# Kernel tuning notes

Hardware: AMD Instinct MI355X
Metric: run time of the kernel (lower is better)

Reference implementation:

```python
import jax, jax.numpy as jnp
import numpy as np

# Model dims (match init_kwargs / input_specs)
T, N, E, F_IN, F_OUT, BW = 16, 50000, 131072, 64, 64, 3


def setup_inputs() -> dict:
    key = jax.random.key(0)
    ks = jax.random.split(key, 6)
    x = jax.random.normal(ks[0], (T, N, F_IN), dtype=jnp.float32)
    M = jax.random.normal(ks[1], (T, T), dtype=jnp.float32)
    adj_rows = jax.random.randint(ks[2], (T, E), 0, N, dtype=jnp.int32)
    adj_cols = jax.random.randint(ks[3], (T, E), 0, N, dtype=jnp.int32)
    adj_vals = jax.random.uniform(ks[4], (T, E), dtype=jnp.float32)
    lim = float(np.sqrt(6.0 / (F_IN + F_OUT)))  # xavier_uniform
    weight = jax.random.uniform(ks[5], (F_IN, F_OUT), minval=-lim, maxval=lim, dtype=jnp.float32)
    return {"x": x, "M": M, "adj_vals": adj_vals, "weight": weight,
            "adj_rows": adj_rows, "adj_cols": adj_cols}


def _spmm(vals, rows, cols, x):
    # COO sparse [N,N] @ dense [N,F]: gather source rows, scatter-add to dest rows.
    return jax.ops.segment_sum(vals[:, None] * x[cols], rows, num_segments=x.shape[0])


def reference(x, M, adj_vals, weight, adj_rows, adj_cols):
    Tn, Nn, F = x.shape
    # Xt = M @ X (full M, as in compute_AtXt)
    Xt = (M @ x.reshape(Tn, -1)).reshape(Tn, Nn, F)
    k_idx = jnp.arange(Tn)
    AtXt = jnp.zeros((Tn, Nn, F), dtype=x.dtype)
    # Banded combination: At[k] = sum_{d=0}^{BW-1, k-d>=0} M[k, k-d] * A[k-d]
    # so At[k] @ Xt[k] = sum_d M[k,k-d] * (A[k-d] @ Xt[k])  -- avoids materializing At.
    for d in range(BW):
        j = k_idx - d
        valid = j >= 0
        jc = jnp.maximum(j, 0)
        w = jnp.where(valid, M[k_idx, jc], 0.0)  # [T] banded weights
        contrib = jax.vmap(_spmm)(adj_vals[jc], adj_rows[jc], adj_cols[jc], Xt)  # [T,N,F]
        AtXt = AtXt + w[:, None, None] * contrib
    # dropout is identity in eval mode; final dense projection
    return AtXt @ weight  # [T, N, F_OUT]
```

## Files before the change

### kernel.cpp

```cpp
#include <hip/hip_runtime.h>

#define TT 16
#define NN 50000
#define FF 64
#define EE 131072
#define NEDGE (TT*EE)
#define RPB 32
#define NRANGE ((NN + RPB - 1) / RPB)
#define NSUB 8
#define BCAP 256
#define NBUCK (NRANGE*NSUB)
#define SLOTS (NSUB*BCAP)
#define EMAX 1791
#define TAILI (EMAX*2)

typedef __attribute__((ext_vector_type(8))) short bf16x8;
typedef __attribute__((ext_vector_type(4))) short bf16x4;
typedef __attribute__((ext_vector_type(4))) float f32x4;
typedef __attribute__((ext_vector_type(2))) int   i32x2;
typedef __attribute__((ext_vector_type(2))) unsigned u32x2;

__device__ __forceinline__ unsigned pack2bf(float a, float b) {
    unsigned ua = __float_as_uint(a) + 0x8000u;
    unsigned ub = __float_as_uint(b) + 0x8000u;
    return __builtin_amdgcn_perm(ub, ua, 0x07060302u);
}
__device__ __forceinline__ float lo16f(unsigned u) { return __uint_as_float(u << 16); }
__device__ __forceinline__ float hi16f(unsigned u) { return __uint_as_float(u & 0xFFFF0000u); }

union U8 { unsigned u[4]; bf16x8 v; };
union U4 { unsigned u[2]; bf16x4 v; };

__device__ __forceinline__ f32x4 mfma16x16x16bf16(bf16x4 a, bf16x4 b, f32x4 c) {
#if __has_builtin(__builtin_amdgcn_mfma_f32_16x16x16bf16_1k)
    return __builtin_amdgcn_mfma_f32_16x16x16bf16_1k(a, b, c, 0, 0, 0);
#elif __has_builtin(__builtin_amdgcn_mfma_f32_16x16x16_bf16)
    return __builtin_amdgcn_mfma_f32_16x16x16_bf16(a, b, c, 0, 0, 0);
#else
    f32x4 d;
    asm volatile("v_mfma_f32_16x16x16_bf16 %0, %1, %2, %3\n\ts_nop 7\n\ts_nop 7"
                 : "=&v"(d) : "v"(a), "v"(b), "v"(c));
    return d;
#endif
}

__global__ __launch_bounds__(256) void k1_proj_mix(
    const float* __restrict__ x, const float* __restrict__ M,
    const float* __restrict__ W, unsigned short* __restrict__ Yt)
{
    const int tid  = threadIdx.x;
    const int wid  = tid >> 6;
    const int lane = tid & 63;
    const int col  = lane & 15;
    const int grp  = lane >> 4;

    bf16x8 bw[2][4];
#pragma unroll
    for (int q = 0; q < 2; ++q)
#pragma unroll
        for (int t = 0; t < 4; ++t) {
            U8 w8;
#pragma unroll
            for (int p = 0; p < 4; ++p)
                w8.u[p] = pack2bf(W[(q*32 + grp*8 + 2*p)*FF + t*16 + col],
                                  W[(q*32 + grp*8 + 2*p + 1)*FF + t*16 + col]);
            bw[q][t] = w8.v;
        }

    U4 m4;
    m4.u[0] = pack2bf(M[col*16 + grp*4 + 0], M[col*16 + grp*4 + 1]);
    m4.u[1] = pack2bf(M[col*16 + grp*4 + 2], M[col*16 + grp*4 + 3]);
    const bf16x4 mf = m4.v;

    const f32x4 zero = {0.f, 0.f, 0.f, 0.f};
    const int nwaves = gridDim.x * 4;
    const size_t lane_off = (size_t)col*NN*FF + grp*8;

    for (int node = blockIdx.x*4 + wid; node < NN; node += 2*nwaves) {
        const int nodeB = node + nwaves;
        const bool hasB = nodeB < NN;

        const float* xa = x + lane_off + (size_t)node*FF;
        f32x4 va0 = __builtin_nontemporal_load(reinterpret_cast<const f32x4*>(xa));
        f32x4 va1 = __builtin_nontemporal_load(reinterpret_cast<const f32x4*>(xa + 4));
        f32x4 va2 = __builtin_nontemporal_load(reinterpret_cast<const f32x4*>(xa + 32));
        f32x4 va3 = __builtin_nontemporal_load(reinterpret_cast<const f32x4*>(xa + 36));
        const float* xb = x + lane_off + (size_t)(hasB ? nodeB : node)*FF;
        f32x4 vb0 = __builtin_nontemporal_load(reinterpret_cast<const f32x4*>(xb));
        f32x4 vb1 = __builtin_nontemporal_load(reinterpret_cast<const f32x4*>(xb + 4));
        f32x4 vb2 = __builtin_nontemporal_load(reinterpret_cast<const f32x4*>(xb + 32));
        f32x4 vb3 = __builtin_nontemporal_load(reinterpret_cast<const f32x4*>(xb + 36));

        {
            U8 a0, a1;
            a0.u[0] = pack2bf(va0[0], va0[1]); a0.u[1] = pack2bf(va0[2], va0[3]);
            a0.u[2] = pack2bf(va1[0], va1[1]); a0.u[3] = pack2bf(va1[2], va1[3]);
            a1.u[0] = pack2bf(va2[0], va2[1]); a1.u[1] = pack2bf(va2[2], va2[3]);
            a1.u[2] = pack2bf(va3[0], va3[1]); a1.u[3] = pack2bf(va3[2], va3[3]);
            f32x4 acc[4];
#pragma unroll
            for (int t = 0; t < 4; ++t) acc[t] = zero;
#pragma unroll
            for (int t = 0; t < 4; ++t)
                acc[t] = __builtin_amdgcn_mfma_f32_16x16x32_bf16(a0.v, bw[0][t], acc[t], 0, 0, 0);
#pragma unroll
            for (int t = 0; t < 4; ++t)
                acc[t] = __builtin_amdgcn_mfma_f32_16x16x32_bf16(a1.v, bw[1][t], acc[t], 0, 0, 0);
#pragma unroll
            for (int t = 0; t < 4; ++t) {
                U4 pb;
                pb.u[0] = pack2bf(acc[t][0], acc[t][1]);
                pb.u[1] = pack2bf(acc[t][2], acc[t][3]);
                f32x4 y = mfma16x16x16bf16(pb.v, mf, zero);
                u32x2 st;
                st[0] = pack2bf(y[0], y[1]);
                st[1] = pack2bf(y[2], y[3]);
                *reinterpret_cast<u32x2*>(Yt + (size_t)node*1024 + col*64 + t*16 + grp*4) = st;
            }
        }
        if (hasB) {
            U8 a0, a1;
            a0.u[0] = pack2bf(vb0[0], vb0[1]); a0.u[1] = pack2bf(vb0[2], vb0[3]);
            a0.u[2] = pack2bf(vb1[0], vb1[1]); a0.u[3] = pack2bf(vb1[2], vb1[3]);
            a1.u[0] = pack2bf(vb2[0], vb2[1]); a1.u[1] = pack2bf(vb2[2], vb2[3]);
            a1.u[2] = pack2bf(vb3[0], vb3[1]); a1.u[3] = pack2bf(vb3[2], vb3[3]);
            f32x4 acc[4];
#pragma unroll
            for (int t = 0; t < 4; ++t) acc[t] = zero;
#pragma unroll
            for (int t = 0; t < 4; ++t)
                acc[t] = __builtin_amdgcn_mfma_f32_16x16x32_bf16(a0.v, bw[0][t], acc[t], 0, 0, 0);
#pragma unroll
            for (int t = 0; t < 4; ++t)
                acc[t] = __builtin_amdgcn_mfma_f32_16x16x32_bf16(a1.v, bw[1][t], acc[t], 0, 0, 0);
#pragma unroll
            for (int t = 0; t < 4; ++t) {
                U4 pb;
                pb.u[0] = pack2bf(acc[t][0], acc[t][1]);
                pb.u[1] = pack2bf(acc[t][2], acc[t][3]);
                f32x4 y = mfma16x16x16bf16(pb.v, mf, zero);
                u32x2 st;
                st[0] = pack2bf(y[0], y[1]);
                st[1] = pack2bf(y[2], y[3]);
                *reinterpret_cast<u32x2*>(Yt + (size_t)nodeB*1024 + col*64 + t*16 + grp*4) = st;
            }
        }
    }
}

__global__ __launch_bounds__(256) void append_kernel(
    const int* __restrict__ rows, const int* __restrict__ cols,
    const float* __restrict__ vals, int* __restrict__ bcnt,
    i32x2* __restrict__ btmp)
{
    const int i = blockIdx.x*256 + threadIdx.x;
    const int r = __builtin_nontemporal_load(rows + i);
    const int j = i >> 17;
    const int b = (r >> 5)*NSUB + (blockIdx.x & 7);
    const int pos = atomicAdd(&bcnt[b], 1);
    if (pos < BCAP) {
        i32x2 e;
        e[0] = __builtin_nontemporal_load(cols + i) | (((r & 31)*16 + j) << 16);
        e[1] = __float_as_int(__builtin_nontemporal_load(vals + i));
        btmp[(size_t)b*BCAP + pos] = e;
    }
}

__global__ __launch_bounds__(256) void sort_kernel(
    const int* __restrict__ bcnt, i32x2* __restrict__ btmp)
{
    __shared__ i32x2 sbuf[SLOTS];
    __shared__ int scnt[512], soff[512], scur[512], pscan[256];

    const int tid = threadIdx.x;
    const int blk = blockIdx.x;
    i32x2* region = btmp + (size_t)blk*SLOTS;

    scnt[tid] = 0; scnt[tid + 256] = 0;
    __syncthreads();

    int bc[NSUB]; i32x2 ent[NSUB];
#pragma unroll
    for (int s = 0; s < NSUB; ++s) {
        int c = bcnt[blk*NSUB + s];
        bc[s] = c < BCAP ? c : BCAP;
    }
#pragma unroll
    for (int s = 0; s < NSUB; ++s)
        if (tid < bc[s]) {
            ent[s] = region[s*BCAP + tid];
            atomicAdd(&scnt[((unsigned)ent[s][0]) >> 16], 1);
        }
    __syncthreads();

    const int a0 = scnt[2*tid], a1 = scnt[2*tid + 1];
    const int ps = a0 + a1;
    pscan[tid] = ps;
    __syncthreads();
    for (int o = 1; o < 256; o <<= 1) {
        int v = (tid >= o) ? pscan[tid - o] : 0;
        __syncthreads();
        pscan[tid] += v;
        __syncthreads();
    }
    const int excl = pscan[tid] - ps;
    soff[2*tid] = excl;      soff[2*tid + 1] = excl + a0;
    scur[2*tid] = excl;      scur[2*tid + 1] = excl + a0;
    __syncthreads();

#pragma unroll
    for (int s = 0; s < NSUB; ++s)
        if (tid < bc[s]) {
            const int key = ((unsigned)ent[s][0]) >> 16;
            const int pos = atomicAdd(&scur[key], 1);
            i32x2 se; se[0] = ent[s][0] & 0xFFFF; se[1] = ent[s][1];
            sbuf[pos] = se;
        }
    __syncthreads();

    const int total = soff[511] + scnt[511];
    const int lim = total < EMAX ? total : EMAX;
    for (int i = tid; i < lim; i += 256) region[i] = sbuf[i];
    int* tail = (int*)region + TAILI;
    tail[tid] = soff[tid];
    tail[tid + 256] = soff[tid + 256];
    if (tid == 0) tail[512] = lim;
}

template<int J>
__device__ __forceinline__ void k2_batch(int p0, int nj, int sbase, int esub, int fq,
    const i32x2* eb, const unsigned short* __restrict__ Yt,
    const float* __restrict__ M, f32x4* acc)
{
    const int p = p0 + esub;
    const bool act = p < nj;
    const int li = act ? (sbase + p) : 0;
    const i32x2 ent = eb[li];
    const float v = act ? __int_as_float(ent[1]) : 0.f;
    const int node = act ? ent[0] : 0;
    const unsigned short* yb = Yt + (size_t)node*1024 + J*64 + fq*4;
    {
        const u32x2 uv = *reinterpret_cast<const u32x2*>(yb);
        const float wv = M[J*17] * v;
        acc[J][0] = fmaf(wv, lo16f(uv[0]), acc[J][0]);
        acc[J][1] = fmaf(wv, hi16f(uv[0]), acc[J][1]);
        acc[J][2] = fmaf(wv, lo16f(uv[1]), acc[J][2]);
        acc[J][3] = fmaf(wv, hi16f(uv[1]), acc[J][3]);
    }
    if constexpr (J < 15) {
        const u32x2 uv = *reinterpret_cast<const u32x2*>(yb + 64);
        const float wv = M[J*17 + 16] * v;
        acc[J+1][0] = fmaf(wv, lo16f(uv[0]), acc[J+1][0]);
        acc[J+1][1] = fmaf(wv, hi16f(uv[0]), acc[J+1][1]);
        acc[J+1][2] = fmaf(wv, lo16f(uv[1]), acc[J+1][2]);
        acc[J+1][3] = fmaf(wv, hi16f(uv[1]), acc[J+1][3]);
    }
    if constexpr (J < 14) {
        const u32x2 uv = *reinterpret_cast<const u32x2*>(yb + 128);
        const float wv = M[J*17 + 32] * v;
        acc[J+2][0] = fmaf(wv, lo16f(uv[0]), acc[J+2][0]);
        acc[J+2][1] = fmaf(wv, hi16f(uv[0]), acc[J+2][1]);
        acc[J+2][2] = fmaf(wv, lo16f(uv[1]), acc[J+2][2]);
        acc[J+2][3] = fmaf(wv, hi16f(uv[1]), acc[J+2][3]);
    }
}

__global__ __launch_bounds__(256) void k2_gather(
    const unsigned short* __restrict__ Yt, const float* __restrict__ M,
    const i32x2* __restrict__ btmp, float* __restrict__ out)
{
    __shared__ i32x2 ebuf[4][128];
    const int tid  = threadIdx.x;
    const int wid  = tid >> 6;
    const int lane = tid & 63;
    const int esub = lane >> 4;
    const int fq   = lane & 15;
    const int r   = blockIdx.x*4 + wid;
    const int blk = r >> 5;
    const int rl  = r & 31;

    const i32x2* region = btmp + (size_t)blk*SLOTS;
    const int* tail = (const int*)region + TAILI;
    int o_l = 0;
    if (lane < 17) o_l = tail[rl*16 + lane];
    int off[17];
#pragma unroll
    for (int j = 0; j < 17; ++j) off[j] = __builtin_amdgcn_readlane(o_l, j);
    int ntot = off[16] - off[0];
    ntot = ntot < 128 ? ntot : 128;
    const i32x2* rowsrc = region + off[0];

    i32x2* eb = ebuf[wid];
    if (lane < ntot)      eb[lane]      = rowsrc[lane];
    if (lane + 64 < ntot) eb[lane + 64] = rowsrc[lane + 64];

    int c[16], sb[16];
#pragma unroll
    for (int j = 0; j < 16; ++j) {
        c[j]  = off[j+1] - off[j];
        sb[j] = off[j] - off[0];
    }

    f32x4 acc[16];
#pragma unroll
    for (int k = 0; k < 16; ++k) acc[k] = (f32x4){0.f, 0.f, 0.f, 0.f};

#define P1(J) k2_batch<J>(0, c[J], sb[J], esub, fq, eb, Yt, M, acc);
    P1(0)  P1(1)  P1(2)  P1(3)  P1(4)  P1(5)  P1(6)  P1(7)
    P1(8)  P1(9)  P1(10) P1(11) P1(12) P1(13) P1(14) P1(15)
#undef P1
#define P2(J) for (int p0 = 4; p0 < c[J]; p0 += 4) \
        k2_batch<J>(p0, c[J], sb[J], esub, fq, eb, Yt, M, acc);
    P2(0)  P2(1)  P2(2)  P2(3)  P2(4)  P2(5)  P2(6)  P2(7)
    P2(8)  P2(9)  P2(10) P2(11) P2(12) P2(13) P2(14) P2(15)
#undef P2

#pragma unroll
    for (int k = 0; k < 16; ++k) {
#pragma unroll
        for (int u = 0; u < 4; ++u) {
            acc[k][u] += __shfl_xor(acc[k][u], 16);
            acc[k][u] += __shfl_xor(acc[k][u], 32);
        }
    }
    if (esub == 0) {
#pragma unroll
        for (int k = 0; k < 16; ++k) {
            *reinterpret_cast<f32x4*>(out + ((size_t)k*NN + r)*FF + fq*4) = acc[k];
        }
    }
}

extern "C" void kernel_launch(void* const* d_in, const int* in_sizes, int n_in,
                              void* d_out, int out_size, void* d_ws, size_t ws_size,
                              hipStream_t stream) {
    (void)in_sizes; (void)n_in; (void)out_size; (void)ws_size;
    const float* x     = (const float*)d_in[0];
    const float* M     = (const float*)d_in[1];
    const float* avals = (const float*)d_in[2];
    const float* W     = (const float*)d_in[3];
    const int*   arows = (const int*)d_in[4];
    const int*   acols = (const int*)d_in[5];
    float* out = (float*)d_out;

    char* ws = (char*)d_ws;
    size_t o = 0;
    unsigned short* Yt = (unsigned short*)(ws + o); o += (size_t)TT*NN*FF*2;
    o = (o + 255) & ~(size_t)255;
    int* bcnt = (int*)(ws + o); o += (size_t)NBUCK*4;  o = (o + 255) & ~(size_t)255;
    i32x2* btmp = (i32x2*)(ws + o);

    (void)hipMemsetAsync(bcnt, 0, (size_t)NBUCK*4, stream);
    hipLaunchKernelGGL(k1_proj_mix, dim3(2048), dim3(256), 0, stream, x, M, W, Yt);
    hipLaunchKernelGGL(append_kernel, dim3(NEDGE/256), dim3(256), 0, stream,
                       arows, acols, avals, bcnt, btmp);
    hipLaunchKernelGGL(sort_kernel, dim3(NRANGE), dim3(256), 0, stream, bcnt, btmp);
    hipLaunchKernelGGL(k2_gather, dim3(12500), dim3(256), 0, stream, Yt, M, btmp, out);
}
```

Baseline: 360.9 us.

## Fuse projection-mix and edge-append kernels into one launch with block ranges

Merges the dense projection/time-mix kernel and the edge bucketing append kernel into one launch, splitting the grid by block index so the two independent workloads can run concurrently. The projection part changes from a grid-stride loop over 2048 blocks to one block per 8 nodes (6250 blocks, two adjacent nodes per wave), with no loop or bounds checks. This removes one launch and the serialization gap between the two kernels, and lets bandwidth-bound dense work overlap atomic-heavy append work. In exchange, per-block setup (loading W and M into registers) is now repeated in many more blocks, and the fused kernel's register footprint applies to the append blocks as well.

```diff
diff --git a/kernel.cpp b/kernel.cpp
--- a/kernel.cpp
+++ b/kernel.cpp
@@ -13,6 +13,8 @@
 #define SLOTS (NSUB*BCAP)
 #define EMAX 1791
 #define TAILI (EMAX*2)
+#define K1BLKS 6250
+#define APPBLKS (NEDGE/256)
 
 typedef __attribute__((ext_vector_type(8))) short bf16x8;
 typedef __attribute__((ext_vector_type(4))) short bf16x4;
@@ -44,59 +46,66 @@
 #endif
 }
 
-__global__ __launch_bounds__(256) void k1_proj_mix(
+__global__ __launch_bounds__(256) void k1_append(
     const float* __restrict__ x, const float* __restrict__ M,
-    const float* __restrict__ W, unsigned short* __restrict__ Yt)
+    const float* __restrict__ W, unsigned short* __restrict__ Yt,
+    const int* __restrict__ rows, const int* __restrict__ cols,
+    const float* __restrict__ vals, int* __restrict__ bcnt,
+    i32x2* __restrict__ btmp)
 {
-    const int tid  = threadIdx.x;
-    const int wid  = tid >> 6;
-    const int lane = tid & 63;
-    const int col  = lane & 15;
-    const int grp  = lane >> 4;
-
-    bf16x8 bw[2][4];
-#pragma unroll
-    for (int q = 0; q < 2; ++q)
-#pragma unroll
-        for (int t = 0; t < 4; ++t) {
-            U8 w8;
-#pragma unroll
-            for (int p = 0; p < 4; ++p)
-                w8.u[p] = pack2bf(W[(q*32 + grp*8 + 2*p)*FF + t*16 + col],
-                                  W[(q*32 + grp*8 + 2*p + 1)*FF + t*16 + col]);
-            bw[q][t] = w8.v;
-        }
-
-    U4 m4;
-    m4.u[0] = pack2bf(M[col*16 + grp*4 + 0], M[col*16 + grp*4 + 1]);
-    m4.u[1] = pack2bf(M[col*16 + grp*4 + 2], M[col*16 + grp*4 + 3]);
-    const bf16x4 mf = m4.v;
-
-    const f32x4 zero = {0.f, 0.f, 0.f, 0.f};
-    const int nwaves = gridDim.x * 4;
-    const size_t lane_off = (size_t)col*NN*FF + grp*8;
-
-    for (int node = blockIdx.x*4 + wid; node < NN; node += 2*nwaves) {
-        const int nodeB = node + nwaves;
-        const bool hasB = nodeB < NN;
+    if (blockIdx.x < K1BLKS) {
+        const int tid  = threadIdx.x;
+        const int wid  = tid >> 6;
+        const int lane = tid & 63;
+        const int col  = lane & 15;
+        const int grp  = lane >> 4;
+
+        bf16x8 bw[2][4];
+#pragma unroll
+        for (int q = 0; q < 2; ++q)
+#pragma unroll
+            for (int t = 0; t < 4; ++t) {
+                U8 w8;
+#pragma unroll
+                for (int p = 0; p < 4; ++p)
+                    w8.u[p] = pack2bf(W[(q*32 + grp*8 + 2*p)*FF + t*16 + col],
+                                      W[(q*32 + grp*8 + 2*p + 1)*FF + t*16 + col]);
+                bw[q][t] = w8.v;
+            }
+
+        U4 m4;
+        m4.u[0] = pack2bf(M[col*16 + grp*4 + 0], M[col*16 + grp*4 + 1]);
+        m4.u[1] = pack2bf(M[col*16 + grp*4 + 2], M[col*16 + grp*4 + 3]);
+        const bf16x4 mf = m4.v;
+
+        const f32x4 zero = {0.f, 0.f, 0.f, 0.f};
+        const int node = (blockIdx.x*4 + wid)*2;
+        const size_t lane_off = (size_t)col*NN*FF + grp*8;
 
         const float* xa = x + lane_off + (size_t)node*FF;
         f32x4 va0 = __builtin_nontemporal_load(reinterpret_cast<const f32x4*>(xa));
         f32x4 va1 = __builtin_nontemporal_load(reinterpret_cast<const f32x4*>(xa + 4));
         f32x4 va2 = __builtin_nontemporal_load(reinterpret_cast<const f32x4*>(xa + 32));
         f32x4 va3 = __builtin_nontemporal_load(reinterpret_cast<const f32x4*>(xa + 36));
-        const float* xb = x + lane_off + (size_t)(hasB ? nodeB : node)*FF;
-        f32x4 vb0 = __builtin_nontemporal_load(reinterpret_cast<const f32x4*>(xb));
-        f32x4 vb1 = __builtin_nontemporal_load(reinterpret_cast<const f32x4*>(xb + 4));
-        f32x4 vb2 = __builtin_nontemporal_load(reinterpret_cast<const f32x4*>(xb + 32));
-        f32x4 vb3 = __builtin_nontemporal_load(reinterpret_cast<const f32x4*>(xb + 36));
-
-        {
+        f32x4 vb0 = __builtin_nontemporal_load(reinterpret_cast<const f32x4*>(xa + 64));
+        f32x4 vb1 = __builtin_nontemporal_load(reinterpret_cast<const f32x4*>(xa + 68));
+        f32x4 vb2 = __builtin_nontemporal_load(reinterpret_cast<const f32x4*>(xa + 96));
+        f32x4 vb3 = __builtin_nontemporal_load(reinterpret_cast<const f32x4*>(xa + 100));
+
+#pragma unroll
+        for (int n2 = 0; n2 < 2; ++n2) {
             U8 a0, a1;
-            a0.u[0] = pack2bf(va0[0], va0[1]); a0.u[1] = pack2bf(va0[2], va0[3]);
-            a0.u[2] = pack2bf(va1[0], va1[1]); a0.u[3] = pack2bf(va1[2], va1[3]);
-            a1.u[0] = pack2bf(va2[0], va2[1]); a1.u[1] = pack2bf(va2[2], va2[3]);
-            a1.u[2] = pack2bf(va3[0], va3[1]); a1.u[3] = pack2bf(va3[2], va3[3]);
+            if (n2 == 0) {
+                a0.u[0] = pack2bf(va0[0], va0[1]); a0.u[1] = pack2bf(va0[2], va0[3]);
+                a0.u[2] = pack2bf(va1[0], va1[1]); a0.u[3] = pack2bf(va1[2], va1[3]);
+                a1.u[0] = pack2bf(va2[0], va2[1]); a1.u[1] = pack2bf(va2[2], va2[3]);
+                a1.u[2] = pack2bf(va3[0], va3[1]); a1.u[3] = pack2bf(va3[2], va3[3]);
+            } else {
+                a0.u[0] = pack2bf(vb0[0], vb0[1]); a0.u[1] = pack2bf(vb0[2], vb0[3]);
+                a0.u[2] = pack2bf(vb1[0], vb1[1]); a0.u[3] = pack2bf(vb1[2], vb1[3]);
+                a1.u[0] = pack2bf(vb2[0], vb2[1]); a1.u[1] = pack2bf(vb2[2], vb2[3]);
+                a1.u[2] = pack2bf(vb3[0], vb3[1]); a1.u[3] = pack2bf(vb3[2], vb3[3]);
+            }
             f32x4 acc[4];
 #pragma unroll
             for (int t = 0; t < 4; ++t) acc[t] = zero;
@@ -115,54 +124,21 @@
                 u32x2 st;
                 st[0] = pack2bf(y[0], y[1]);
                 st[1] = pack2bf(y[2], y[3]);
-                *reinterpret_cast<u32x2*>(Yt + (size_t)node*1024 + col*64 + t*16 + grp*4) = st;
+                *reinterpret_cast<u32x2*>(Yt + (size_t)(node + n2)*1024 + col*64 + t*16 + grp*4) = st;
             }
         }
-        if (hasB) {
-            U8 a0, a1;
-            a0.u[0] = pack2bf(vb0[0], vb0[1]); a0.u[1] = pack2bf(vb0[2], vb0[3]);
-            a0.u[2] = pack2bf(vb1[0], vb1[1]); a0.u[3] = pack2bf(vb1[2], vb1[3]);
-            a1.u[0] = pack2bf(vb2[0], vb2[1]); a1.u[1] = pack2bf(vb2[2], vb2[3]);
-            a1.u[2] = pack2bf(vb3[0], vb3[1]); a1.u[3] = pack2bf(vb3[2], vb3[3]);
-            f32x4 acc[4];
-#pragma unroll
-            for (int t = 0; t < 4; ++t) acc[t] = zero;
-#pragma unroll
-            for (int t = 0; t < 4; ++t)
-                acc[t] = __builtin_amdgcn_mfma_f32_16x16x32_bf16(a0.v, bw[0][t], acc[t], 0, 0, 0);
-#pragma unroll
-            for (int t = 0; t < 4; ++t)
-                acc[t] = __builtin_amdgcn_mfma_f32_16x16x32_bf16(a1.v, bw[1][t], acc[t], 0, 0, 0);
-#pragma unroll
-            for (int t = 0; t < 4; ++t) {
-                U4 pb;
-                pb.u[0] = pack2bf(acc[t][0], acc[t][1]);
-                pb.u[1] = pack2bf(acc[t][2], acc[t][3]);
-                f32x4 y = mfma16x16x16bf16(pb.v, mf, zero);
-                u32x2 st;
-                st[0] = pack2bf(y[0], y[1]);
-                st[1] = pack2bf(y[2], y[3]);
-                *reinterpret_cast<u32x2*>(Yt + (size_t)nodeB*1024 + col*64 + t*16 + grp*4) = st;
-            }
-        }
-    }
-}
-
-__global__ __launch_bounds__(256) void append_kernel(
-    const int* __restrict__ rows, const int* __restrict__ cols,
-    const float* __restrict__ vals, int* __restrict__ bcnt,
-    i32x2* __restrict__ btmp)
-{
-    const int i = blockIdx.x*256 + threadIdx.x;
-    const int r = __builtin_nontemporal_load(rows + i);
-    const int j = i >> 17;
-    const int b = (r >> 5)*NSUB + (blockIdx.x & 7);
-    const int pos = atomicAdd(&bcnt[b], 1);
-    if (pos < BCAP) {
-        i32x2 e;
-        e[0] = __builtin_nontemporal_load(cols + i) | (((r & 31)*16 + j) << 16);
-        e[1] = __float_as_int(__builtin_nontemporal_load(vals + i));
-        btmp[(size_t)b*BCAP + pos] = e;
+    } else {
+        const int i = (blockIdx.x - K1BLKS)*256 + threadIdx.x;
+        const int r = __builtin_nontemporal_load(rows + i);
+        const int j = i >> 17;
+        const int b = (r >> 5)*NSUB + (blockIdx.x & 7);
+        const int pos = atomicAdd(&bcnt[b], 1);
+        if (pos < BCAP) {
+            i32x2 e;
+            e[0] = __builtin_nontemporal_load(cols + i) | (((r & 31)*16 + j) << 16);
+            e[1] = __float_as_int(__builtin_nontemporal_load(vals + i));
+            btmp[(size_t)b*BCAP + pos] = e;
+        }
     }
 }
 
@@ -351,9 +327,8 @@
     i32x2* btmp = (i32x2*)(ws + o);
 
     (void)hipMemsetAsync(bcnt, 0, (size_t)NBUCK*4, stream);
-    hipLaunchKernelGGL(k1_proj_mix, dim3(2048), dim3(256), 0, stream, x, M, W, Yt);
-    hipLaunchKernelGGL(append_kernel, dim3(NEDGE/256), dim3(256), 0, stream,
-                       arows, acols, avals, bcnt, btmp);
+    hipLaunchKernelGGL(k1_append, dim3(K1BLKS + APPBLKS), dim3(256), 0, stream,
+                       x, M, W, Yt, arows, acols, avals, bcnt, btmp);
     hipLaunchKernelGGL(sort_kernel, dim3(NRANGE), dim3(256), 0, stream, bcnt, btmp);
     hipLaunchKernelGGL(k2_gather, dim3(12500), dim3(256), 0, stream, Yt, M, btmp, out);
 }
```

Result: faster. 349.8 us (-3.1%).
